# Performance work log

Measured on AMD Instinct MI355X. Metric: run time of the kernel, lower is better.

Reference implementation:

```python
import jax, jax.numpy as jnp
import numpy as np

B, S, D = 2, 2048, 1024
H, DK = 16, 64  # num_heads, key_dim (value_dim defaults to key_dim)


def setup_inputs() -> dict:
    key = jax.random.key(0)
    ks = jax.random.split(key, 11)
    init = lambda k, shape, fan_in: jax.random.uniform(
        k, shape, jnp.float32, -1.0, 1.0) * (1.0 / np.sqrt(fan_in))
    return {
        "query": jax.random.normal(ks[0], (B, S, D), jnp.float32),
        "key": jax.random.normal(ks[1], (B, S, D), jnp.float32),
        "value": jax.random.normal(ks[2], (B, S, D), jnp.float32),
        "Wq": init(ks[3], (D, H, DK), D),
        "bq": jnp.zeros((H, DK), jnp.float32),
        "Wk": init(ks[4], (D, H, DK), D),
        "bk": jnp.zeros((H, DK), jnp.float32),
        "Wv": init(ks[5], (D, H, DK), D),
        "bv": jnp.zeros((H, DK), jnp.float32),
        "Wo": init(ks[6], (H, DK, D), H * DK),
        "bo": jnp.zeros((D,), jnp.float32),
    }


def reference(query, key, value, Wq, bq, Wk, bk, Wv, bv, Wo, bo):
    # QKV projections: abc,cde->abde (EinsumDense with bias on (H, DK))
    q = jnp.einsum("bsd,dhk->bshk", query, Wq) + bq  # [B,S,H,DK]
    k = jnp.einsum("bsd,dhk->bshk", key, Wk) + bk
    v = jnp.einsum("bsd,dhk->bshk", value, Wv) + bv
    # Keras scales the query before the dot product
    q = q * (1.0 / jnp.sqrt(jnp.asarray(DK, q.dtype)))
    # aecd,abcd->acbe : [B,H,Sq,Sk]
    scores = jnp.einsum("bqhk,bshk->bhqs", q, k)
    probs = jax.nn.softmax(scores, axis=-1)
    # acbe,aecd->abcd : [B,Sq,H,DK]
    attn = jnp.einsum("bhqs,bshk->bqhk", probs, v)
    # output projection: abcd,cde->abe
    out = jnp.einsum("bqhk,hkd->bqd", attn, Wo) + bo  # [B,S,D]
    return out
```

## Files before the change

### kernel.cpp

```cpp
#include <hip/hip_runtime.h>
#include <hip/hip_bf16.h>
#include <stdint.h>
#include <stddef.h>


typedef __bf16 bf16;
typedef __attribute__((ext_vector_type(4))) bf16 bf16x4;
typedef __attribute__((ext_vector_type(8))) bf16 bf16x8;
typedef __attribute__((ext_vector_type(4))) float f32x4;
typedef __attribute__((ext_vector_type(16))) float f32x16;
typedef __attribute__((ext_vector_type(2))) unsigned int uint2v;

#define DEVINL static __device__ __forceinline__

DEVINL void gload_lds16(const void* g, void* l) {
  __builtin_amdgcn_global_load_lds(
      (const __attribute__((address_space(1))) void*)g,
      (__attribute__((address_space(3))) void*)l, 16, 0, 0);
}

DEVINL f32x4 mfma16(bf16x8 a, bf16x8 b, f32x4 c) {
  return __builtin_amdgcn_mfma_f32_16x16x32_bf16(a, b, c, 0, 0, 0);
}
DEVINL f32x16 mfma32(bf16x8 a, bf16x8 b, f32x16 c) {
  return __builtin_amdgcn_mfma_f32_32x32x16_bf16(a, b, c, 0, 0, 0);
}
DEVINL unsigned pack2(float lo, float hi) {
  union { bf16 h[2]; unsigned u; } t;
  t.h[0] = (bf16)lo; t.h[1] = (bf16)hi;
  return t.u;
}
DEVINL bf16x8 mk8(unsigned a, unsigned b, unsigned c, unsigned d) {
  union { unsigned u[4]; bf16x8 v; } t;
  t.u[0] = a; t.u[1] = b; t.u[2] = c; t.u[3] = d;
  return t.v;
}

__global__ __launch_bounds__(256) void wt_kernel(
    const float* __restrict__ w0, const float* __restrict__ w1,
    const float* __restrict__ w2, const float* __restrict__ w3,
    bf16* __restrict__ out) {
  __shared__ float tile[64 * 65];
  int t = blockIdx.y;
  const float* w = (t == 0) ? w0 : (t == 1) ? w1 : (t == 2) ? w2 : w3;
  bf16* o = out + (size_t)t * 1024 * 1024;
  int tb = blockIdx.x;
  int k0 = (tb >> 4) * 64, n0 = (tb & 15) * 64;
  int c = threadIdx.x & 63, r0 = threadIdx.x >> 6;
  for (int r = r0; r < 64; r += 4)
    tile[r * 65 + c] = w[(size_t)(k0 + r) * 1024 + n0 + c];
  __syncthreads();
  for (int r = r0; r < 64; r += 4)
    o[(size_t)(n0 + r) * 1024 + k0 + c] = (bf16)tile[c * 65 + r];
}

__global__ __launch_bounds__(256) void gemm_qkv(
    const float* __restrict__ Aq, const float* __restrict__ Ak,
    const float* __restrict__ Av, const bf16* __restrict__ Wt,
    const float* __restrict__ bq, const float* __restrict__ bk,
    const float* __restrict__ bv,
    bf16* __restrict__ outQ, bf16* __restrict__ outK, bf16* __restrict__ Vt) {
  int z = blockIdx.z;
  const float* A   = (z == 0) ? Aq : (z == 1) ? Ak : Av;
  const bf16* Wz   = Wt + (size_t)z * 1024 * 1024;
  const float* bia = (z == 0) ? bq : (z == 1) ? bk : bv;
  float scale      = (z == 0) ? 0.125f : 1.0f;

  __shared__ bf16 As[2][128 * 32];
  __shared__ bf16 Bs[2][128 * 32];

  int m0 = blockIdx.x * 128, n0 = blockIdx.y * 128;
  int tid = threadIdx.x, w = tid >> 6, l = tid & 63;
  int wm = (w >> 1) * 64, wn = (w & 1) * 64;
  int c16 = l & 15, g = l >> 4;
  int rsw = (c16 >> 1) & 3;
  int ar = tid >> 1, akb = (tid & 1) * 16;
  int asw = (ar >> 1) & 3;
  int as0 = (((akb >> 3) + 0) ^ asw) * 8;
  int as1 = (((akb >> 3) + 1) ^ asw) * 8;

  int brow0 = (w * 2 + 0) * 16 + (l >> 2);
  int brow1 = (w * 2 + 1) * 16 + (l >> 2);
  int bk0 = ((l & 3) ^ ((brow0 >> 1) & 3)) * 8;
  int bk1 = ((l & 3) ^ ((brow1 >> 1) & 3)) * 8;

  f32x4 acc[4][4] = {};

#define STAGE_B(buf, kt)                                                     \
  do {                                                                       \
    gload_lds16(Wz + (size_t)(n0 + brow0) * 1024 + (kt) + bk0,               \
                (char*)Bs[buf] + (w * 2 + 0) * 1024 + l * 16);               \
    gload_lds16(Wz + (size_t)(n0 + brow1) * 1024 + (kt) + bk1,               \
                (char*)Bs[buf] + (w * 2 + 1) * 1024 + l * 16);               \
  } while (0)

#define PACK_A(buf)                                                          \
  do {                                                                       \
    bf16x8 h0, h1;                                                           \
    _Pragma("unroll") for (int j = 0; j < 4; ++j) {                          \
      h0[j] = (bf16)f0[j]; h0[4 + j] = (bf16)f1[j];                          \
      h1[j] = (bf16)f2[j]; h1[4 + j] = (bf16)f3[j];                          \
    }                                                                        \
    *(bf16x8*)&As[buf][ar * 32 + as0] = h0;                                  \
    *(bf16x8*)&As[buf][ar * 32 + as1] = h1;                                  \
  } while (0)

  STAGE_B(0, 0);
  {
    const float* ap = A + (size_t)(m0 + ar) * 1024 + akb;
    f32x4 f0 = *(const f32x4*)(ap + 0);
    f32x4 f1 = *(const f32x4*)(ap + 4);
    f32x4 f2 = *(const f32x4*)(ap + 8);
    f32x4 f3 = *(const f32x4*)(ap + 12);
    PACK_A(0);
  }
  __syncthreads();

  int cur = 0;
  for (int kt = 0; kt < 1024; kt += 32) {
    f32x4 f0, f1, f2, f3;
    if (kt < 992) {
      STAGE_B(cur ^ 1, kt + 32);
      const float* ap = A + (size_t)(m0 + ar) * 1024 + kt + 32 + akb;
      f0 = *(const f32x4*)(ap + 0);
      f1 = *(const f32x4*)(ap + 4);
      f2 = *(const f32x4*)(ap + 8);
      f3 = *(const f32x4*)(ap + 12);
    }
    bf16x8 af[4], bfr[4];
#pragma unroll
    for (int mt = 0; mt < 4; ++mt)
      af[mt] = *(const bf16x8*)&As[cur][(wm + mt * 16 + c16) * 32 + ((g ^ rsw) * 8)];
#pragma unroll
    for (int nt = 0; nt < 4; ++nt)
      bfr[nt] = *(const bf16x8*)&Bs[cur][(wn + nt * 16 + c16) * 32 + ((g ^ rsw) * 8)];
#pragma unroll
    for (int mt = 0; mt < 4; ++mt)
#pragma unroll
      for (int nt = 0; nt < 4; ++nt)
        acc[mt][nt] = mfma16(af[mt], bfr[nt], acc[mt][nt]);
    if (kt < 992) PACK_A(cur ^ 1);
    __syncthreads();
    cur ^= 1;
  }
#undef STAGE_B
#undef PACK_A

  if (z < 2) {
    bf16* Cout = (z == 0) ? outQ : outK;
#pragma unroll
    for (int mt = 0; mt < 4; ++mt)
#pragma unroll
      for (int nt = 0; nt < 4; ++nt) {
        int n = n0 + wn + nt * 16 + c16;
        float bb = bia[n];
#pragma unroll
        for (int r = 0; r < 4; ++r) {
          int m = m0 + wm + mt * 16 + g * 4 + r;
          Cout[(size_t)m * 1024 + n] = (bf16)((acc[mt][nt][r] + bb) * scale);
        }
      }
  } else {
#pragma unroll
    for (int mt = 0; mt < 4; ++mt)
#pragma unroll
      for (int nt = 0; nt < 4; ++nt) {
        int n = n0 + wn + nt * 16 + c16;
        float bb = bia[n];
        int m = m0 + wm + mt * 16 + g * 4;
        int b = m >> 11, s = m & 2047;
        bf16x4 v;
#pragma unroll
        for (int r = 0; r < 4; ++r) v[r] = (bf16)(acc[mt][nt][r] + bb);
        *(bf16x4*)&Vt[((size_t)(b * 16 + (n >> 6)) * 64 + (n & 63)) * 2048 + s] = v;
      }
  }
}

__global__ __launch_bounds__(256) void flash_kernel(
    const bf16* __restrict__ Qp, const bf16* __restrict__ Kp,
    const bf16* __restrict__ Vt, bf16* __restrict__ AO) {
  __shared__ __align__(16) bf16 Ks[2][64 * 64];
  __shared__ __align__(16) bf16 Vs[2][64 * 64];

  int orig = blockIdx.x;
  int wg = (orig & 7) * 64 + (orig >> 3);
  int bh = wg >> 4, qb = wg & 15;
  int b = bh >> 4, h = bh & 15;
  int tid = threadIdx.x, w = tid >> 6, l = tid & 63;
  int lo5 = l & 31, g = l >> 5;
  int q0 = qb * 128 + w * 32;

  const bf16* qptr = Qp + (size_t)(b * 2048 + q0 + lo5) * 1024 + h * 64 + g * 8;
  bf16x8 qf0 = *(const bf16x8*)(qptr + 0);
  bf16x8 qf1 = *(const bf16x8*)(qptr + 16);
  bf16x8 qf2 = *(const bf16x8*)(qptr + 32);
  bf16x8 qf3 = *(const bf16x8*)(qptr + 48);

  const bf16* kbase = Kp + (size_t)(b * 2048) * 1024 + h * 64;
  const bf16* vbase = Vt + (size_t)bh * 64 * 2048;

  int u0 = w * 64 + l;
  int u1 = (4 + w) * 64 + l;
  int r0s = u0 >> 3, c0s = (u0 & 7) ^ (r0s & 7);
  int r1s = u1 >> 3, c1s = (u1 & 7) ^ (r1s & 7);

#define STAGE(buf, s0)                                                          \
  do {                                                                          \
    gload_lds16(kbase + (size_t)((s0) + r0s) * 1024 + c0s * 8,                  \
                (bf16*)Ks[buf] + u0 * 8);                                       \
    gload_lds16(kbase + (size_t)((s0) + r1s) * 1024 + c1s * 8,                  \
                (bf16*)Ks[buf] + u1 * 8);                                       \
    gload_lds16(vbase + (size_t)r0s * 2048 + (s0) + c0s * 8,                    \
                (bf16*)Vs[buf] + u0 * 8);                                       \
    gload_lds16(vbase + (size_t)r1s * 2048 + (s0) + c1s * 8,                    \
                (bf16*)Vs[buf] + u1 * 8);                                       \
  } while (0)

#define LDSK(cp, nt, kt) \
  (*(const bf16x8*)&cp[(((nt)*32 + lo5) << 6) + (((((kt)*2 + g)) ^ (lo5 & 7)) << 3)])
#define LDSV(cp, dt, st) \
  (*(const bf16x8*)&cp[(((dt)*32 + lo5) << 6) + (((((st)*2 + g)) ^ (lo5 & 7)) << 3)])

  f32x16 o0 = {}, o1 = {};
  float ps0 = 0.f, ps1 = 0.f, ps2 = 0.f, ps3 = 0.f;

  STAGE(0, 0);
  int cur = 0;
  for (int t = 0; t < 32; ++t) {
    if (t < 31) {
      STAGE(cur ^ 1, (t + 1) * 64);
      asm volatile("s_waitcnt vmcnt(4)" ::: "memory");
    } else {
      asm volatile("s_waitcnt vmcnt(0)" ::: "memory");
    }
    __builtin_amdgcn_s_barrier();
    __builtin_amdgcn_sched_barrier(0);
    const bf16* kc = Ks[cur];
    const bf16* vc = Vs[cur];

    f32x16 sv = {};
    sv = mfma32(LDSK(kc, 0, 0), qf0, sv);
    sv = mfma32(LDSK(kc, 0, 1), qf1, sv);
    sv = mfma32(LDSK(kc, 0, 2), qf2, sv);
    sv = mfma32(LDSK(kc, 0, 3), qf3, sv);
    float p[16];
#pragma unroll
    for (int r = 0; r < 16; ++r) p[r] = __expf(sv[r]);
    ps0 += p[0] + p[4] + p[8] + p[12];
    ps1 += p[1] + p[5] + p[9] + p[13];
    ps2 += p[2] + p[6] + p[10] + p[14];
    ps3 += p[3] + p[7] + p[11] + p[15];
    unsigned pw0 = pack2(p[0], p[1]), pw1 = pack2(p[2], p[3]);
    unsigned pw2 = pack2(p[4], p[5]), pw3 = pack2(p[6], p[7]);
    unsigned pw4 = pack2(p[8], p[9]), pw5 = pack2(p[10], p[11]);
    unsigned pw6 = pack2(p[12], p[13]), pw7 = pack2(p[14], p[15]);
    uint2v a02 = __builtin_amdgcn_permlane32_swap(pw0, pw2, false, false);
    uint2v a13 = __builtin_amdgcn_permlane32_swap(pw1, pw3, false, false);
    uint2v a46 = __builtin_amdgcn_permlane32_swap(pw4, pw6, false, false);
    uint2v a57 = __builtin_amdgcn_permlane32_swap(pw5, pw7, false, false);
    bf16x8 pa0 = mk8(a02.x, a13.x, a02.y, a13.y);
    bf16x8 pa1 = mk8(a46.x, a57.x, a46.y, a57.y);

    f32x16 sw = {};
    sw = mfma32(LDSK(kc, 1, 0), qf0, sw);
    sw = mfma32(LDSK(kc, 1, 1), qf1, sw);
    sw = mfma32(LDSK(kc, 1, 2), qf2, sw);
    sw = mfma32(LDSK(kc, 1, 3), qf3, sw);
#pragma unroll
    for (int r = 0; r < 16; ++r) p[r] = __expf(sw[r]);
    ps0 += p[0] + p[4] + p[8] + p[12];
    ps1 += p[1] + p[5] + p[9] + p[13];
    ps2 += p[2] + p[6] + p[10] + p[14];
    ps3 += p[3] + p[7] + p[11] + p[15];
    pw0 = pack2(p[0], p[1]); pw1 = pack2(p[2], p[3]);
    pw2 = pack2(p[4], p[5]); pw3 = pack2(p[6], p[7]);
    pw4 = pack2(p[8], p[9]); pw5 = pack2(p[10], p[11]);
    pw6 = pack2(p[12], p[13]); pw7 = pack2(p[14], p[15]);
    a02 = __builtin_amdgcn_permlane32_swap(pw0, pw2, false, false);
    a13 = __builtin_amdgcn_permlane32_swap(pw1, pw3, false, false);
    a46 = __builtin_amdgcn_permlane32_swap(pw4, pw6, false, false);
    a57 = __builtin_amdgcn_permlane32_swap(pw5, pw7, false, false);
    bf16x8 pb0 = mk8(a02.x, a13.x, a02.y, a13.y);
    bf16x8 pb1 = mk8(a46.x, a57.x, a46.y, a57.y);

    o0 = mfma32(pa0, LDSV(vc, 0, 0), o0);
    o1 = mfma32(pa0, LDSV(vc, 1, 0), o1);
    o0 = mfma32(pa1, LDSV(vc, 0, 1), o0);
    o1 = mfma32(pa1, LDSV(vc, 1, 1), o1);
    o0 = mfma32(pb0, LDSV(vc, 0, 2), o0);
    o1 = mfma32(pb0, LDSV(vc, 1, 2), o1);
    o0 = mfma32(pb1, LDSV(vc, 0, 3), o0);
    o1 = mfma32(pb1, LDSV(vc, 1, 3), o1);

    __builtin_amdgcn_sched_barrier(0);
    __builtin_amdgcn_s_barrier();
    cur ^= 1;
  }
#undef STAGE
#undef LDSK
#undef LDSV

  float plsum = (ps0 + ps1) + (ps2 + ps3);
  float tot = plsum + __shfl_xor(plsum, 32);

#pragma unroll
  for (int r = 0; r < 16; ++r) {
    int qr = (r & 3) + 8 * (r >> 2) + 4 * g;
    float inv = 1.0f / __shfl(tot, qr);
    bf16* op = AO + (size_t)(b * 2048 + q0 + qr) * 1024 + h * 64 + lo5;
    op[0]  = (bf16)(o0[r] * inv);
    op[32] = (bf16)(o1[r] * inv);
  }
}

__global__ __launch_bounds__(256) void gemm_o(
    const bf16* __restrict__ A, const bf16* __restrict__ Wt3,
    const float* __restrict__ bo, float* __restrict__ C) {
  __shared__ bf16 As[2][128 * 32];
  __shared__ bf16 Bs[2][128 * 32];
  int m0 = blockIdx.x * 128, n0 = blockIdx.y * 128;
  int tid = threadIdx.x, w = tid >> 6, l = tid & 63;
  int wm = (w >> 1) * 64, wn = (w & 1) * 64;
  int c16 = l & 15, g = l >> 4;
  int rsw = (c16 >> 1) & 3;

  int brow0 = (w * 2 + 0) * 16 + (l >> 2);
  int brow1 = (w * 2 + 1) * 16 + (l >> 2);
  int bk0 = ((l & 3) ^ ((brow0 >> 1) & 3)) * 8;
  int bk1 = ((l & 3) ^ ((brow1 >> 1) & 3)) * 8;

  f32x4 acc[4][4] = {};

#define STAGE_O(buf, kt)                                                     \
  do {                                                                       \
    gload_lds16(A + (size_t)(m0 + brow0) * 1024 + (kt) + bk0,                \
                (char*)As[buf] + (w * 2 + 0) * 1024 + l * 16);               \
    gload_lds16(A + (size_t)(m0 + brow1) * 1024 + (kt) + bk1,                \
                (char*)As[buf] + (w * 2 + 1) * 1024 + l * 16);               \
    gload_lds16(Wt3 + (size_t)(n0 + brow0) * 1024 + (kt) + bk0,              \
                (char*)Bs[buf] + (w * 2 + 0) * 1024 + l * 16);               \
    gload_lds16(Wt3 + (size_t)(n0 + brow1) * 1024 + (kt) + bk1,              \
                (char*)Bs[buf] + (w * 2 + 1) * 1024 + l * 16);               \
  } while (0)

  STAGE_O(0, 0);
  __syncthreads();

  int cur = 0;
  for (int kt = 0; kt < 1024; kt += 32) {
    if (kt < 992) STAGE_O(cur ^ 1, kt + 32);
    bf16x8 af[4], bfr[4];
#pragma unroll
    for (int mt = 0; mt < 4; ++mt)
      af[mt] = *(const bf16x8*)&As[cur][(wm + mt * 16 + c16) * 32 + ((g ^ rsw) * 8)];
#pragma unroll
    for (int nt = 0; nt < 4; ++nt)
      bfr[nt] = *(const bf16x8*)&Bs[cur][(wn + nt * 16 + c16) * 32 + ((g ^ rsw) * 8)];
#pragma unroll
    for (int mt = 0; mt < 4; ++mt)
#pragma unroll
      for (int nt = 0; nt < 4; ++nt)
        acc[mt][nt] = mfma16(af[mt], bfr[nt], acc[mt][nt]);
    __syncthreads();
    cur ^= 1;
  }
#undef STAGE_O

#pragma unroll
  for (int mt = 0; mt < 4; ++mt)
#pragma unroll
    for (int nt = 0; nt < 4; ++nt) {
      int n = n0 + wn + nt * 16 + c16;
      float bb = bo[n];
#pragma unroll
      for (int r = 0; r < 4; ++r) {
        int m = m0 + wm + mt * 16 + g * 4 + r;
        C[(size_t)m * 1024 + n] = acc[mt][nt][r] + bb;
      }
    }
}

extern "C" void kernel_launch(void* const* d_in, const int* in_sizes, int n_in,
                              void* d_out, int out_size, void* d_ws, size_t ws_size,
                              hipStream_t stream) {
  const float* query = (const float*)d_in[0];
  const float* key_  = (const float*)d_in[1];
  const float* value = (const float*)d_in[2];
  const float* Wq = (const float*)d_in[3];
  const float* bq = (const float*)d_in[4];
  const float* Wk = (const float*)d_in[5];
  const float* bk = (const float*)d_in[6];
  const float* Wv = (const float*)d_in[7];
  const float* bv = (const float*)d_in[8];
  const float* Wo = (const float*)d_in[9];
  const float* bo = (const float*)d_in[10];
  float* out = (float*)d_out;

  char* ws = (char*)d_ws;
  const size_t MB = 1024 * 1024;
  bf16* Wt = (bf16*)(ws);
  bf16* Qp = (bf16*)(ws + 8 * MB);
  bf16* Kp = (bf16*)(ws + 16 * MB);
  bf16* Vt = (bf16*)(ws + 24 * MB);
  bf16* AO = (bf16*)(ws + 32 * MB);

  dim3 blk(256);
  wt_kernel<<<dim3(256, 4), blk, 0, stream>>>(Wq, Wk, Wv, Wo, Wt);
  gemm_qkv<<<dim3(32, 8, 3), blk, 0, stream>>>(query, key_, value, Wt,
                                               bq, bk, bv, Qp, Kp, Vt);
  flash_kernel<<<dim3(512), blk, 0, stream>>>(Qp, Kp, Vt, AO);
  gemm_o<<<dim3(32, 8), blk, 0, stream>>>(AO, Wt + (size_t)3 * 1024 * 1024, bo, out);
}
```

Baseline: 129.5 us.

## Deepen QKV/out-proj GEMM pipelining with manual waitcnts and use raw exp2 in softmax

The QKV projection GEMM is restructured into a two-stage unrolled loop that keeps two register sets of prefetched fp32 A tiles in flight, with explicit vmcnt/lgkmcnt waits and raw barriers replacing __syncthreads. The output projection loop likewise uses partial vmcnt waits so the next tile's loads stay outstanding across the barrier. The attention softmax replaces __expf with a direct v_exp_f32 (base-2), and the log2(e) factor is folded into the query scale. The aim is to hide global load latency and cut exp instruction count. In exchange the hand-counted waitcnts are fragile and could cause races if the counts are wrong.

```diff
diff --git a/kernel.cpp b/kernel.cpp
--- a/kernel.cpp
+++ b/kernel.cpp
@@ -24,6 +24,11 @@
 }
 DEVINL f32x16 mfma32(bf16x8 a, bf16x8 b, f32x16 c) {
   return __builtin_amdgcn_mfma_f32_32x32x16_bf16(a, b, c, 0, 0, 0);
+}
+DEVINL float fexp2(float x) {
+  float r;
+  asm("v_exp_f32 %0, %1" : "=v"(r) : "v"(x));
+  return r;
 }
 DEVINL unsigned pack2(float lo, float hi) {
   union { bf16 h[2]; unsigned u; } t;
@@ -64,7 +69,7 @@
   const float* A   = (z == 0) ? Aq : (z == 1) ? Ak : Av;
   const bf16* Wz   = Wt + (size_t)z * 1024 * 1024;
   const float* bia = (z == 0) ? bq : (z == 1) ? bk : bv;
-  float scale      = (z == 0) ? 0.125f : 1.0f;
+  float scale      = (z == 0) ? 0.18033688011112042f : 1.0f;
 
   __shared__ bf16 As[2][128 * 32];
   __shared__ bf16 Bs[2][128 * 32];
@@ -85,6 +90,7 @@
   int bk1 = ((l & 3) ^ ((brow1 >> 1) & 3)) * 8;
 
   f32x4 acc[4][4] = {};
+  f32x4 rA0[4], rA1[4];
 
 #define STAGE_B(buf, kt)                                                     \
   do {                                                                       \
@@ -94,57 +100,79 @@
                 (char*)Bs[buf] + (w * 2 + 1) * 1024 + l * 16);               \
   } while (0)
 
-#define PACK_A(buf)                                                          \
+#define LOADA(dst, kt)                                                       \
+  do {                                                                       \
+    const float* ap_ = A + (size_t)(m0 + ar) * 1024 + (kt) + akb;            \
+    dst[0] = *(const f32x4*)(ap_ + 0);                                       \
+    dst[1] = *(const f32x4*)(ap_ + 4);                                       \
+    dst[2] = *(const f32x4*)(ap_ + 8);                                       \
+    dst[3] = *(const f32x4*)(ap_ + 12);                                      \
+  } while (0)
+
+#define PACK_A(buf, src)                                                     \
   do {                                                                       \
     bf16x8 h0, h1;                                                           \
     _Pragma("unroll") for (int j = 0; j < 4; ++j) {                          \
-      h0[j] = (bf16)f0[j]; h0[4 + j] = (bf16)f1[j];                          \
-      h1[j] = (bf16)f2[j]; h1[4 + j] = (bf16)f3[j];                          \
+      h0[j] = (bf16)src[0][j]; h0[4 + j] = (bf16)src[1][j];                  \
+      h1[j] = (bf16)src[2][j]; h1[4 + j] = (bf16)src[3][j];                  \
     }                                                                        \
     *(bf16x8*)&As[buf][ar * 32 + as0] = h0;                                  \
     *(bf16x8*)&As[buf][ar * 32 + as1] = h1;                                  \
   } while (0)
 
+#define COMPUTE(buf)                                                         \
+  do {                                                                       \
+    bf16x8 af[4], bfr[4];                                                    \
+    _Pragma("unroll") for (int mt = 0; mt < 4; ++mt)                         \
+      af[mt] = *(const bf16x8*)&As[buf][(wm + mt * 16 + c16) * 32 +          \
+                                        ((g ^ rsw) * 8)];                    \
+    _Pragma("unroll") for (int nt = 0; nt < 4; ++nt)                         \
+      bfr[nt] = *(const bf16x8*)&Bs[buf][(wn + nt * 16 + c16) * 32 +         \
+                                         ((g ^ rsw) * 8)];                   \
+    _Pragma("unroll") for (int mt = 0; mt < 4; ++mt)                         \
+      _Pragma("unroll") for (int nt = 0; nt < 4; ++nt)                       \
+        acc[mt][nt] = mfma16(af[mt], bfr[nt], acc[mt][nt]);                  \
+  } while (0)
+
   STAGE_B(0, 0);
-  {
-    const float* ap = A + (size_t)(m0 + ar) * 1024 + akb;
-    f32x4 f0 = *(const f32x4*)(ap + 0);
-    f32x4 f1 = *(const f32x4*)(ap + 4);
-    f32x4 f2 = *(const f32x4*)(ap + 8);
-    f32x4 f3 = *(const f32x4*)(ap + 12);
-    PACK_A(0);
-  }
+  LOADA(rA0, 0);
+  PACK_A(0, rA0);
+  LOADA(rA1, 32);
   __syncthreads();
 
-  int cur = 0;
-  for (int kt = 0; kt < 1024; kt += 32) {
-    f32x4 f0, f1, f2, f3;
-    if (kt < 992) {
-      STAGE_B(cur ^ 1, kt + 32);
-      const float* ap = A + (size_t)(m0 + ar) * 1024 + kt + 32 + akb;
-      f0 = *(const f32x4*)(ap + 0);
-      f1 = *(const f32x4*)(ap + 4);
-      f2 = *(const f32x4*)(ap + 8);
-      f3 = *(const f32x4*)(ap + 12);
+  for (int t = 0; t < 32; t += 2) {
+    STAGE_B(1, (t + 1) * 32);
+    if (t < 30) LOADA(rA0, (t + 2) * 32);
+    if (t == 30) { asm volatile("s_waitcnt vmcnt(6)" ::: "memory"); }
+    else         { asm volatile("s_waitcnt vmcnt(10)" ::: "memory"); }
+    __builtin_amdgcn_s_barrier();
+    __builtin_amdgcn_sched_barrier(0);
+    COMPUTE(0);
+    PACK_A(1, rA1);
+    asm volatile("s_waitcnt lgkmcnt(0)" ::: "memory");
+    __builtin_amdgcn_sched_barrier(0);
+    __builtin_amdgcn_s_barrier();
+    if (t < 30) {
+      STAGE_B(0, (t + 2) * 32);
+      LOADA(rA1, (t + 3) * 32);
+      asm volatile("s_waitcnt vmcnt(10)" ::: "memory");
+    } else {
+      asm volatile("s_waitcnt vmcnt(0)" ::: "memory");
     }
-    bf16x8 af[4], bfr[4];
-#pragma unroll
-    for (int mt = 0; mt < 4; ++mt)
-      af[mt] = *(const bf16x8*)&As[cur][(wm + mt * 16 + c16) * 32 + ((g ^ rsw) * 8)];
-#pragma unroll
-    for (int nt = 0; nt < 4; ++nt)
-      bfr[nt] = *(const bf16x8*)&Bs[cur][(wn + nt * 16 + c16) * 32 + ((g ^ rsw) * 8)];
-#pragma unroll
-    for (int mt = 0; mt < 4; ++mt)
-#pragma unroll
-      for (int nt = 0; nt < 4; ++nt)
-        acc[mt][nt] = mfma16(af[mt], bfr[nt], acc[mt][nt]);
-    if (kt < 992) PACK_A(cur ^ 1);
-    __syncthreads();
-    cur ^= 1;
+    __builtin_amdgcn_s_barrier();
+    __builtin_amdgcn_sched_barrier(0);
+    COMPUTE(1);
+    if (t < 30) {
+      PACK_A(0, rA0);
+      asm volatile("s_waitcnt lgkmcnt(0)" ::: "memory");
+    }
+    __builtin_amdgcn_sched_barrier(0);
+    __builtin_amdgcn_s_barrier();
   }
 #undef STAGE_B
+#undef LOADA
 #undef PACK_A
+#undef COMPUTE
 
   if (z < 2) {
     bf16* Cout = (z == 0) ? outQ : outK;
@@ -246,7 +274,7 @@
     sv = mfma32(LDSK(kc, 0, 3), qf3, sv);
     float p[16];
 #pragma unroll
-    for (int r = 0; r < 16; ++r) p[r] = __expf(sv[r]);
+    for (int r = 0; r < 16; ++r) p[r] = fexp2(sv[r]);
     ps0 += p[0] + p[4] + p[8] + p[12];
     ps1 += p[1] + p[5] + p[9] + p[13];
     ps2 += p[2] + p[6] + p[10] + p[14];
@@ -268,7 +296,7 @@
     sw = mfma32(LDSK(kc, 1, 2), qf2, sw);
     sw = mfma32(LDSK(kc, 1, 3), qf3, sw);
 #pragma unroll
-    for (int r = 0; r < 16; ++r) p[r] = __expf(sw[r]);
+    for (int r = 0; r < 16; ++r) p[r] = fexp2(sw[r]);
     ps0 += p[0] + p[4] + p[8] + p[12];
     ps1 += p[1] + p[5] + p[9] + p[13];
     ps2 += p[2] + p[6] + p[10] + p[14];
@@ -348,8 +376,15 @@
   __syncthreads();
 
   int cur = 0;
-  for (int kt = 0; kt < 1024; kt += 32) {
-    if (kt < 992) STAGE_O(cur ^ 1, kt + 32);
+  for (int t = 0; t < 32; ++t) {
+    if (t < 31) {
+      STAGE_O(cur ^ 1, (t + 1) * 32);
+      asm volatile("s_waitcnt vmcnt(4)" ::: "memory");
+    } else {
+      asm volatile("s_waitcnt vmcnt(0)" ::: "memory");
+    }
+    __builtin_amdgcn_s_barrier();
+    __builtin_amdgcn_sched_barrier(0);
     bf16x8 af[4], bfr[4];
 #pragma unroll
     for (int mt = 0; mt < 4; ++mt)
@@ -362,7 +397,8 @@
 #pragma unroll
       for (int nt = 0; nt < 4; ++nt)
         acc[mt][nt] = mfma16(af[mt], bfr[nt], acc[mt][nt]);
-    __syncthreads();
+    __builtin_amdgcn_sched_barrier(0);
+    __builtin_amdgcn_s_barrier();
     cur ^= 1;
   }
 #undef STAGE_O
```

Measured after the change: 146.4 us. +13.1%, slower.
